# Kernel tuning notes

Hardware: AMD Instinct MI355X
Metric: run time of the kernel (lower is better)

Reference implementation:

```python
import jax, jax.numpy as jnp
import numpy as np

B, N, H = 8, 256, 256


def setup_inputs() -> dict:
    key = jax.random.key(0)
    ks = jax.random.split(key, 6)
    s = 1.0 / np.sqrt(H)
    return {
        "x": jax.random.normal(ks[0], (B, N, H), dtype=jnp.float32),
        "edge_gate": jax.random.uniform(ks[1], (B, N, N, H), dtype=jnp.float32),
        "U_w": jax.random.uniform(ks[2], (H, H), jnp.float32, -s, s),
        "U_b": jax.random.uniform(ks[3], (H,), jnp.float32, -s, s),
        "V_w": jax.random.uniform(ks[4], (H, H), jnp.float32, -s, s),
        "V_b": jax.random.uniform(ks[5], (H,), jnp.float32, -s, s),
    }


def reference(x, edge_gate, U_w, U_b, V_w, V_b):
    # Ux, Vx: (B, N, H); torch Linear computes x @ W.T + b
    Ux = jnp.einsum("bnh,kh->bnk", x, U_w) + U_b
    Vx = jnp.einsum("bnh,kh->bnk", x, V_w) + V_b
    # sum_j edge_gate[b,i,j,h] * Vx[b,j,h]  -> (B, N, H), fused (no gateVx materialized)
    num = jnp.einsum("bijh,bjh->bih", edge_gate, Vx)
    denom = 1e-20 + jnp.sum(edge_gate, axis=2)  # (B, N, H)
    return Ux + num / denom
```

## Files before the change

kernel.cpp:

```cpp
#include <hip/hip_runtime.h>


typedef float f4 __attribute__((ext_vector_type(4)));
typedef float f2 __attribute__((ext_vector_type(2)));

#define S36 36

__global__ __launch_bounds__(256) void gemm_uv(
    const float* __restrict__ x, const float* __restrict__ U_w,
    const float* __restrict__ U_b, const float* __restrict__ V_w,
    const float* __restrict__ V_b, float* __restrict__ Ux,
    float* __restrict__ Vx) {
  __shared__ float Xs[64 * S36];
  __shared__ float Ws[32 * S36];
  const int t  = threadIdx.x;
  const int gx = blockIdx.x;
  const int gy = blockIdx.y;
  const int m0 = gy * 64;
  const bool isU = (gx < 8);
  const float* Wsrc = isU ? U_w : V_w;
  const float* bsrc = isU ? U_b : V_b;
  const int n0 = (gx & 7) * 32;
  float* dst = isU ? Ux : Vx;

  const int tn = t & 15;
  const int tm = t >> 4;
  float acc[4][2] = {};

  const int lm = t >> 3;
  const int lc = t & 7;

  for (int k0 = 0; k0 < 256; k0 += 32) {
    #pragma unroll
    for (int r = 0; r < 2; ++r) {
      const int m = r * 32 + lm;
      f4 v = *(const f4*)(x + (m0 + m) * 256 + k0 + lc * 4);
      *(f4*)(&Xs[m * S36 + lc * 4]) = v;
    }
    {
      f4 v = *(const f4*)(Wsrc + (n0 + lm) * 256 + k0 + lc * 4);
      *(f4*)(&Ws[lm * S36 + lc * 4]) = v;
    }
    __syncthreads();
    #pragma unroll
    for (int kq = 0; kq < 8; ++kq) {
      f4 a0 = *(const f4*)(&Xs[(tm * 4 + 0) * S36 + kq * 4]);
      f4 a1 = *(const f4*)(&Xs[(tm * 4 + 1) * S36 + kq * 4]);
      f4 a2 = *(const f4*)(&Xs[(tm * 4 + 2) * S36 + kq * 4]);
      f4 a3 = *(const f4*)(&Xs[(tm * 4 + 3) * S36 + kq * 4]);
      f4 b0 = *(const f4*)(&Ws[(tn * 2 + 0) * S36 + kq * 4]);
      f4 b1 = *(const f4*)(&Ws[(tn * 2 + 1) * S36 + kq * 4]);
      acc[0][0] += a0.x*b0.x + a0.y*b0.y + a0.z*b0.z + a0.w*b0.w;
      acc[0][1] += a0.x*b1.x + a0.y*b1.y + a0.z*b1.z + a0.w*b1.w;
      acc[1][0] += a1.x*b0.x + a1.y*b0.y + a1.z*b0.z + a1.w*b0.w;
      acc[1][1] += a1.x*b1.x + a1.y*b1.y + a1.z*b1.z + a1.w*b1.w;
      acc[2][0] += a2.x*b0.x + a2.y*b0.y + a2.z*b0.z + a2.w*b0.w;
      acc[2][1] += a2.x*b1.x + a2.y*b1.y + a2.z*b1.z + a2.w*b1.w;
      acc[3][0] += a3.x*b0.x + a3.y*b0.y + a3.z*b0.z + a3.w*b0.w;
      acc[3][1] += a3.x*b1.x + a3.y*b1.y + a3.z*b1.z + a3.w*b1.w;
    }
    __syncthreads();
  }

  const float bb0 = bsrc[n0 + 2 * tn + 0];
  const float bb1 = bsrc[n0 + 2 * tn + 1];
  #pragma unroll
  for (int i = 0; i < 4; ++i) {
    f2 o;
    o.x = acc[i][0] + bb0;
    o.y = acc[i][1] + bb1;
    *(f2*)(dst + (m0 + 4 * tm + i) * 256 + n0 + 2 * tn) = o;
  }
}

__global__ __launch_bounds__(256, 4) void fuse_gate(
    const float* __restrict__ eg, const float* __restrict__ Vx,
    float* __restrict__ out) {
  const int i  = blockIdx.x;
  const int b  = blockIdx.y;
  const int t  = threadIdx.x;
  const int h4 = t & 63;
  const int jg = t >> 6;

  const f4* eg4 = (const f4*)eg;
  const f4* vx4 = (const f4*)Vx;
  const int row = b * 256 + i;
  const int egb = row * (256 * 64);
  const int vxb = b * (256 * 64);

  f4 num = {0.f, 0.f, 0.f, 0.f};
  f4 den = {0.f, 0.f, 0.f, 0.f};
  #pragma unroll 8
  for (int j = jg; j < 256; j += 4) {
    f4 e = __builtin_nontemporal_load(&eg4[egb + j * 64 + h4]);
    f4 v = vx4[vxb + j * 64 + h4];
    num += e * v;
    den += e;
  }

  __shared__ f4 nsh[256];
  __shared__ f4 dsh[256];
  nsh[t] = num;
  dsh[t] = den;
  __syncthreads();

  if (t < 64) {
    f4 ns = nsh[t];
    f4 ds = dsh[t];
    #pragma unroll
    for (int g = 1; g < 4; ++g) { ns += nsh[g * 64 + t]; ds += dsh[g * 64 + t]; }
    f4 u = ((const f4*)out)[row * 64 + t];
    f4 eps = {1e-20f, 1e-20f, 1e-20f, 1e-20f};
    f4 o = u + ns / (eps + ds);
    ((f4*)out)[row * 64 + t] = o;
  }
}

extern "C" void kernel_launch(void* const* d_in, const int* in_sizes, int n_in,
                              void* d_out, int out_size, void* d_ws, size_t ws_size,
                              hipStream_t stream) {
  const float* x   = (const float*)d_in[0];
  const float* eg  = (const float*)d_in[1];
  const float* U_w = (const float*)d_in[2];
  const float* U_b = (const float*)d_in[3];
  const float* V_w = (const float*)d_in[4];
  const float* V_b = (const float*)d_in[5];
  float* out = (float*)d_out;
  float* Vx  = (float*)d_ws;

  gemm_uv<<<dim3(16, 32), 256, 0, stream>>>(x, U_w, U_b, V_w, V_b, out, Vx);
  fuse_gate<<<dim3(256, 8), 256, 0, stream>>>(eg, Vx, out);
}
```

Before: 683.6 us.

## Assign one wavefront per output row in gate reduction, drop LDS reduction

```diff
diff --git a/kernel.cpp b/kernel.cpp
--- a/kernel.cpp
+++ b/kernel.cpp
@@ -73,47 +73,57 @@
   }
 }
 
-__global__ __launch_bounds__(256, 4) void fuse_gate(
+__global__ __launch_bounds__(256) void fuse_gate(
     const float* __restrict__ eg, const float* __restrict__ Vx,
     float* __restrict__ out) {
-  const int i  = blockIdx.x;
-  const int b  = blockIdx.y;
-  const int t  = threadIdx.x;
-  const int h4 = t & 63;
-  const int jg = t >> 6;
+  const int t    = threadIdx.x;
+  const int lane = t & 63;
+  const int w    = t >> 6;
+  const int row  = blockIdx.x * 4 + w;
+  const int b    = row >> 8;
 
-  const f4* eg4 = (const f4*)eg;
-  const f4* vx4 = (const f4*)Vx;
-  const int row = b * 256 + i;
-  const int egb = row * (256 * 64);
-  const int vxb = b * (256 * 64);
+  const f4* eg4 = (const f4*)eg + (size_t)row * (256 * 64) + lane;
+  const f4* vx4 = (const f4*)Vx + (size_t)b   * (256 * 64) + lane;
 
-  f4 num = {0.f, 0.f, 0.f, 0.f};
-  f4 den = {0.f, 0.f, 0.f, 0.f};
-  #pragma unroll 8
-  for (int j = jg; j < 256; j += 4) {
-    f4 e = __builtin_nontemporal_load(&eg4[egb + j * 64 + h4]);
-    f4 v = vx4[vxb + j * 64 + h4];
-    num += e * v;
-    den += e;
+  f4 n0 = {0.f, 0.f, 0.f, 0.f}, n1 = {0.f, 0.f, 0.f, 0.f};
+  f4 d0 = {0.f, 0.f, 0.f, 0.f}, d1 = {0.f, 0.f, 0.f, 0.f};
+
+  #pragma unroll 1
+  for (int j = 0; j < 256; j += 8) {
+    const f4* ep = eg4 + j * 64;
+    const f4* vp = vx4 + j * 64;
+    f4 e0 = __builtin_nontemporal_load(ep + 0 * 64);
+    f4 e1 = __builtin_nontemporal_load(ep + 1 * 64);
+    f4 e2 = __builtin_nontemporal_load(ep + 2 * 64);
+    f4 e3 = __builtin_nontemporal_load(ep + 3 * 64);
+    f4 e4 = __builtin_nontemporal_load(ep + 4 * 64);
+    f4 e5 = __builtin_nontemporal_load(ep + 5 * 64);
+    f4 e6 = __builtin_nontemporal_load(ep + 6 * 64);
+    f4 e7 = __builtin_nontemporal_load(ep + 7 * 64);
+    f4 v0 = vp[0 * 64];
+    f4 v1 = vp[1 * 64];
+    f4 v2 = vp[2 * 64];
+    f4 v3 = vp[3 * 64];
+    f4 v4 = vp[4 * 64];
+    f4 v5 = vp[5 * 64];
+    f4 v6 = vp[6 * 64];
+    f4 v7 = vp[7 * 64];
+    n0 += e0 * v0;  d0 += e0;
+    n1 += e1 * v1;  d1 += e1;
+    n0 += e2 * v2;  d0 += e2;
+    n1 += e3 * v3;  d1 += e3;
+    n0 += e4 * v4;  d0 += e4;
+    n1 += e5 * v5;  d1 += e5;
+    n0 += e6 * v6;  d0 += e6;
+    n1 += e7 * v7;  d1 += e7;
   }
 
-  __shared__ f4 nsh[256];
-  __shared__ f4 dsh[256];
-  nsh[t] = num;
-  dsh[t] = den;
-  __syncthreads();
-
-  if (t < 64) {
-    f4 ns = nsh[t];
-    f4 ds = dsh[t];
-    #pragma unroll
-    for (int g = 1; g < 4; ++g) { ns += nsh[g * 64 + t]; ds += dsh[g * 64 + t]; }
-    f4 u = ((const f4*)out)[row * 64 + t];
-    f4 eps = {1e-20f, 1e-20f, 1e-20f, 1e-20f};
-    f4 o = u + ns / (eps + ds);
-    ((f4*)out)[row * 64 + t] = o;
-  }
+  const f4 num = n0 + n1;
+  const f4 den = d0 + d1;
+  const size_t o = (size_t)row * 64 + lane;
+  f4 u = ((const f4*)out)[o];
+  f4 eps = {1e-20f, 1e-20f, 1e-20f, 1e-20f};
+  ((f4*)out)[o] = u + num / (eps + den);
 }
 
 extern "C" void kernel_launch(void* const* d_in, const int* in_sizes, int n_in,
@@ -129,5 +139,5 @@
   float* Vx  = (float*)d_ws;
 
   gemm_uv<<<dim3(16, 32), 256, 0, stream>>>(x, U_w, U_b, V_w, V_b, out, Vx);
-  fuse_gate<<<dim3(256, 8), 256, 0, stream>>>(eg, Vx, out);
+  fuse_gate<<<dim3(512), 256, 0, stream>>>(eg, Vx, out);
 }
```

New measurement: 668.1 us. 2.3% less time.
